# Performance work log

Hardware: AMD Instinct MI355X
Metric: run time of the kernel (lower is better)

Reference implementation:

```python
import jax, jax.numpy as jnp
import numpy as np

D_MODEL = 768
D_FF = 3072
N_HEADS = 12
HEAD_DIM = D_MODEL // N_HEADS
SUB_SCALE = 0.5
LN_EPS = 1e-5


def _layer_norm(x, g, b):
    mu = jnp.mean(x, axis=-1, keepdims=True)
    var = jnp.var(x, axis=-1, keepdims=True)
    return (x - mu) * jax.lax.rsqrt(var + LN_EPS) * g + b


def setup_inputs() -> dict:
    key = jax.random.key(0)
    ks = jax.random.split(key, 12)
    B, T = 1, 4096
    s = lambda fan_in: 1.0 / np.sqrt(fan_in)
    return {
        "x": jax.random.normal(ks[0], (B, T, D_MODEL), dtype=jnp.float32),
        "ln1_g": jnp.ones((D_MODEL,), jnp.float32),
        "ln1_b": jnp.zeros((D_MODEL,), jnp.float32),
        "ln2_g": jnp.ones((D_MODEL,), jnp.float32),
        "ln2_b": jnp.zeros((D_MODEL,), jnp.float32),
        "qkv_w": jax.random.normal(ks[1], (D_MODEL, 3 * D_MODEL), jnp.float32) * s(D_MODEL),
        "qkv_b": jnp.zeros((3 * D_MODEL,), jnp.float32),
        "out_w": jax.random.normal(ks[2], (D_MODEL, D_MODEL), jnp.float32) * s(D_MODEL),
        "out_b": jnp.zeros((D_MODEL,), jnp.float32),
        "fc1_w": jax.random.normal(ks[3], (D_MODEL, D_FF), jnp.float32) * s(D_MODEL),
        "fc1_b": jnp.zeros((D_FF,), jnp.float32),
        "fc2_w": jax.random.normal(ks[4], (D_FF, D_MODEL), jnp.float32) * s(D_FF),
        "fc2_b": jnp.zeros((D_MODEL,), jnp.float32),
    }


def reference(x, ln1_g, ln1_b, ln2_g, ln2_b, qkv_w, qkv_b, out_w, out_b,
              fc1_w, fc1_b, fc2_w, fc2_b):
    B, T, C = x.shape
    # --- attention sub-block ---
    h = _layer_norm(x, ln1_g, ln1_b) * SUB_SCALE
    qkv = h @ qkv_w + qkv_b                      # [B,T,3C]
    q, k, v = jnp.split(qkv, 3, axis=-1)
    split = lambda t: t.reshape(B, T, N_HEADS, HEAD_DIM).transpose(0, 2, 1, 3)
    q, k, v = split(q), split(k), split(v)       # [B,H,T,Hd]
    scores = jnp.einsum('bhqd,bhkd->bhqk', q, k) / jnp.sqrt(jnp.float32(HEAD_DIM))
    weights = jax.nn.softmax(scores, axis=-1)    # [B,H,T,T] (no mask, as in source)
    attn = jnp.einsum('bhqk,bhkd->bhqd', weights, v)
    attn = attn.transpose(0, 2, 1, 3).reshape(B, T, C)
    x = x + attn @ out_w + out_b
    # --- MLP sub-block ---
    h2 = _layer_norm(x, ln2_g, ln2_b) * SUB_SCALE
    h2 = jax.nn.gelu(h2 @ fc1_w + fc1_b, approximate=False)  # nn.GELU() = exact erf
    h2 = h2 @ fc2_w + fc2_b
    return x + h2
```

## Files before the change

kernel.cpp:

```cpp
#include <hip/hip_runtime.h>
#include <hip/hip_bf16.h>
#include <math.h>

#define TSEQ 4096
#define DMODEL 768
#define DFF 3072
#define NHEADS 12
#define HDIM 64

typedef __attribute__((ext_vector_type(8))) short short8;
typedef __attribute__((ext_vector_type(4))) float f32x4;
typedef unsigned short ushort;
typedef unsigned int uint;

typedef __attribute__((address_space(1))) ushort as1_ushort;
typedef __attribute__((address_space(3))) ushort as3_ushort;

__device__ __forceinline__ void gl_lds16(const ushort* g, const ushort* l) {
    __builtin_amdgcn_global_load_lds((as1_ushort*)(uintptr_t)g,
                                     (as3_ushort*)(uint)(uintptr_t)l, 16, 0, 0);
}

__device__ __forceinline__ ushort f2bf(float f) {
    union { float f; unsigned i; } c; c.f = f;
    unsigned x = c.i;
    unsigned r = x + 0x7FFFu + ((x >> 16) & 1u);
    return (ushort)(r >> 16);
}
__device__ __forceinline__ float asf(uint u) {
    union { unsigned i; float f; } c; c.i = u; return c.f;
}
__device__ __forceinline__ float gelu_fast(float v) {
    float y = v * (0.7978845608f + 0.03567740814f * v * v);
    float u = exp2f(y * -2.8853900817779268f);
    float r;
    asm("v_rcp_f32 %0, %1" : "=v"(r) : "v"(1.f + u));
    return v * r;
}

__global__ __launch_bounds__(256) void ln_half_kernel(
    const float* __restrict__ x, const float* __restrict__ g,
    const float* __restrict__ b, ushort* __restrict__ out)
{
    int row = blockIdx.x;
    const float* xr = x + (size_t)row * DMODEL;
    float v[3];
    float s = 0.f, s2 = 0.f;
    #pragma unroll
    for (int i = 0; i < 3; i++) {
        v[i] = xr[threadIdx.x + 256 * i];
        s += v[i]; s2 += v[i] * v[i];
    }
    #pragma unroll
    for (int m = 1; m < 64; m <<= 1) { s += __shfl_xor(s, m, 64); s2 += __shfl_xor(s2, m, 64); }
    __shared__ float ss[4], ss2[4];
    int wid = threadIdx.x >> 6;
    if ((threadIdx.x & 63) == 0) { ss[wid] = s; ss2[wid] = s2; }
    __syncthreads();
    s = ss[0] + ss[1] + ss[2] + ss[3];
    s2 = ss2[0] + ss2[1] + ss2[2] + ss2[3];
    float mu = s * (1.f / DMODEL);
    float var = s2 * (1.f / DMODEL) - mu * mu;
    float rs = rsqrtf(var + 1e-5f);
    #pragma unroll
    for (int i = 0; i < 3; i++) {
        int c = threadIdx.x + 256 * i;
        float h = (v[i] - mu) * rs * g[c] + b[c];
        out[(size_t)row * DMODEL + c] = f2bf(h * 0.5f);
    }
}

__global__ __launch_bounds__(256) void transpose_cast_kernel(
    const float* __restrict__ in, ushort* __restrict__ out, int K, int N)
{
    __shared__ float tile[32][33];
    int k0 = blockIdx.x * 32, n0 = blockIdx.y * 32;
    int c = threadIdx.x & 31, r0 = threadIdx.x >> 5;
    #pragma unroll
    for (int i = 0; i < 4; i++) {
        int r = r0 + i * 8;
        tile[r][c] = in[(size_t)(k0 + r) * N + n0 + c];
    }
    __syncthreads();
    #pragma unroll
    for (int i = 0; i < 4; i++) {
        int r = r0 + i * 8;
        out[(size_t)(n0 + r) * K + k0 + c] = f2bf(tile[c][r]);
    }
}

template<int EPI>
__global__ __launch_bounds__(256) void gemm_kernel(
    const ushort* __restrict__ A, const ushort* __restrict__ Bt,
    const float* __restrict__ bias, const float* __restrict__ res,
    void* __restrict__ out, ushort* __restrict__ vTout, int M, int N, int K)
{
    __shared__ ushort As[2][128 * 32];
    __shared__ ushort Bs[2][128 * 32];
    int bm = blockIdx.x * 128, bn = blockIdx.y * 128;
    int tid = threadIdx.x;
    int wid = tid >> 6, lane = tid & 63;
    int wm = (wid >> 1) * 64, wn = (wid & 1) * 64;
    int lg = lane >> 4, lr = lane & 15;
    int srow = lane >> 2, scol = (lane & 3) * 8;
    f32x4 acc[4][4] = {};

    const ushort* ga0 = A  + (size_t)(bm + wid * 16 + srow) * K + scol;
    const ushort* ga1 = A  + (size_t)(bm + 64 + wid * 16 + srow) * K + scol;
    const ushort* gb0 = Bt + (size_t)(bn + wid * 16 + srow) * K + scol;
    const ushort* gb1 = Bt + (size_t)(bn + 64 + wid * 16 + srow) * K + scol;

    gl_lds16(ga0, &As[0][wid * 512]);
    gl_lds16(ga1, &As[0][2048 + wid * 512]);
    gl_lds16(gb0, &Bs[0][wid * 512]);
    gl_lds16(gb1, &Bs[0][2048 + wid * 512]);

    int nt = K >> 5;
    for (int t = 0; t < nt; t++) {
        int cur = t & 1;
        __syncthreads();
        if (t + 1 < nt) {
            int k0 = (t + 1) << 5;
            int nb = cur ^ 1;
            gl_lds16(ga0 + k0, &As[nb][wid * 512]);
            gl_lds16(ga1 + k0, &As[nb][2048 + wid * 512]);
            gl_lds16(gb0 + k0, &Bs[nb][wid * 512]);
            gl_lds16(gb1 + k0, &Bs[nb][2048 + wid * 512]);
        }
        short8 a[4], b[4];
        #pragma unroll
        for (int mi = 0; mi < 4; mi++) a[mi] = *(const short8*)&As[cur][(wm + mi * 16 + lr) * 32 + lg * 8];
        #pragma unroll
        for (int ni = 0; ni < 4; ni++) b[ni] = *(const short8*)&Bs[cur][(wn + ni * 16 + lr) * 32 + lg * 8];
        #pragma unroll
        for (int mi = 0; mi < 4; mi++)
            #pragma unroll
            for (int ni = 0; ni < 4; ni++)
                acc[mi][ni] = __builtin_amdgcn_mfma_f32_16x16x32_bf16(a[mi], b[ni], acc[mi][ni], 0, 0, 0);
    }

    #pragma unroll
    for (int mi = 0; mi < 4; mi++) {
        #pragma unroll
        for (int ni = 0; ni < 4; ni++) {
            int col = bn + wn + ni * 16 + lr;
            float bv = bias[col];
            if (EPI == 3 && bn >= 1536) {
                int row0 = bm + wm + mi * 16 + lg * 4;
                uint2 pk;
                pk.x = (uint)f2bf(acc[mi][ni][0] + bv) | ((uint)f2bf(acc[mi][ni][1] + bv) << 16);
                pk.y = (uint)f2bf(acc[mi][ni][2] + bv) | ((uint)f2bf(acc[mi][ni][3] + bv) << 16);
                *(uint2*)&vTout[(size_t)(col - 1536) * TSEQ + row0] = pk;
            } else {
                #pragma unroll
                for (int r = 0; r < 4; r++) {
                    int row = bm + wm + mi * 16 + lg * 4 + r;
                    float v = acc[mi][ni][r] + bv;
                    size_t idx = (size_t)row * N + col;
                    if (EPI == 1) {
                        ((ushort*)out)[idx] = f2bf(gelu_fast(v));
                    } else if (EPI == 2) {
                        ((float*)out)[idx] = v + res[idx];
                    } else {
                        ((ushort*)out)[idx] = f2bf(v);
                    }
                }
            }
        }
    }
}

template<int EPI>
__global__ __launch_bounds__(256) void gemm_64_kernel(
    const ushort* __restrict__ A, const ushort* __restrict__ Bt,
    const float* __restrict__ bias, const float* __restrict__ res,
    void* __restrict__ out, int M, int N, int K)
{
    __shared__ ushort As[2][64 * 32];
    __shared__ ushort Bs[2][64 * 32];
    int bm = blockIdx.x * 64, bn = blockIdx.y * 64;
    int tid = threadIdx.x;
    int wid = tid >> 6, lane = tid & 63;
    int wm = (wid >> 1) * 32, wn = (wid & 1) * 32;
    int lg = lane >> 4, lr = lane & 15;
    int srow = tid >> 2;
    int sunit = (tid & 3) ^ (srow & 3);
    f32x4 acc[2][2] = {};

    const ushort* ga = A  + (size_t)(bm + srow) * K + sunit * 8;
    const ushort* gb = Bt + (size_t)(bn + srow) * K + sunit * 8;

    gl_lds16(ga, &As[0][tid * 8]);
    gl_lds16(gb, &Bs[0][tid * 8]);

    int nt = K >> 5;
    for (int t = 0; t < nt; t++) {
        int cur = t & 1;
        __syncthreads();
        if (t + 1 < nt) {
            int k0 = (t + 1) << 5;
            int nb = cur ^ 1;
            gl_lds16(ga + k0, &As[nb][tid * 8]);
            gl_lds16(gb + k0, &Bs[nb][tid * 8]);
        }
        short8 a[2], b[2];
        #pragma unroll
        for (int mi = 0; mi < 2; mi++) {
            int row = wm + mi * 16 + lr;
            a[mi] = *(const short8*)&As[cur][row * 32 + ((lg ^ (row & 3)) * 8)];
        }
        #pragma unroll
        for (int ni = 0; ni < 2; ni++) {
            int row = wn + ni * 16 + lr;
            b[ni] = *(const short8*)&Bs[cur][row * 32 + ((lg ^ (row & 3)) * 8)];
        }
        #pragma unroll
        for (int mi = 0; mi < 2; mi++)
            #pragma unroll
            for (int ni = 0; ni < 2; ni++)
                acc[mi][ni] = __builtin_amdgcn_mfma_f32_16x16x32_bf16(a[mi], b[ni], acc[mi][ni], 0, 0, 0);
    }

    #pragma unroll
    for (int mi = 0; mi < 2; mi++) {
        #pragma unroll
        for (int ni = 0; ni < 2; ni++) {
            int col = bn + wn + ni * 16 + lr;
            float bv = bias[col];
            #pragma unroll
            for (int r = 0; r < 4; r++) {
                int row = bm + wm + mi * 16 + lg * 4 + r;
                float v = acc[mi][ni][r] + bv;
                size_t idx = (size_t)row * N + col;
                if (EPI == 0) {
                    ((ushort*)out)[idx] = f2bf(v);
                } else if (EPI == 1) {
                    ((ushort*)out)[idx] = f2bf(gelu_fast(v));
                } else {
                    ((float*)out)[idx] = v + res[idx];
                }
            }
        }
    }
}

__global__ __launch_bounds__(512) void attn_kernel(
    const ushort* __restrict__ qkv, const ushort* __restrict__ vT,
    ushort* __restrict__ Opart, float* __restrict__ ml)
{
    int combo = blockIdx.x % 48;
    int qblk  = blockIdx.x / 48;
    int h     = combo >> 2;
    int split = combo & 3;
    __shared__ ushort smem[16384 + 256 * 40];
    ushort* Ps = smem + 16384;
    int tid = threadIdx.x, wid = tid >> 6, lane = tid & 63;
    int lg = lane >> 4, lr = lane & 15;
    const float C1 = 0.18033688011112042f;
    const float KC = 12.0f * C1;
    int x7 = lr & 7;

    {
        int row = tid >> 1;
        int u0 = (tid & 1) * 4;
        int r7 = row & 7;
        const ushort* src = qkv + (size_t)(qblk * 256 + row) * 2304 + h * HDIM;
        #pragma unroll
        for (int i = 0; i < 4; i++) {
            int u = u0 + i;
            *(short8*)&smem[row * 64 + ((u ^ r7) * 8)] = *(const short8*)(src + (size_t)(u * 8));
        }
    }
    int q0row = (wid * 32 + lr) * 64;
    int q1row = q0row + 16 * 64;
    short8 qa0 = *(const short8*)&smem[q0row + (lg ^ x7) * 8];
    short8 qa1 = *(const short8*)&smem[q0row + ((4 + lg) ^ x7) * 8];
    short8 qb0 = *(const short8*)&smem[q1row + (lg ^ x7) * 8];
    short8 qb1 = *(const short8*)&smem[q1row + ((4 + lg) ^ x7) * 8];
    __syncthreads();

    short8 vone;
    #pragma unroll
    for (int i = 0; i < 8; i++) vone[i] = (short)0x3F80;

    int krow = tid >> 3;
    int kunit = (tid & 7) ^ (krow & 7);
    const ushort* kg = qkv + (size_t)(split * 1024 + krow) * 2304 + DMODEL + h * HDIM + kunit * 8;
    const ushort* vgp = vT + (size_t)(h * HDIM + krow) * TSEQ + split * 1024 + kunit * 8;

    gl_lds16(kg, &smem[tid * 8]);
    gl_lds16(vgp, &smem[8192 + tid * 8]);
    kg += 64 * 2304;
    vgp += 64;

    f32x4 o0[4] = {}, o1[4] = {};
    f32x4 s0sum = {}, s1sum = {};
    const int NT = 16;
    int prow0 = (wid * 32 + lr) * 40;
    int prow1 = prow0 + 16 * 40;

    for (int kt = 0; kt < NT; kt++) {
        int cur = kt & 1, nb = cur ^ 1;
        __syncthreads();
        if (kt + 1 < NT) {
            gl_lds16(kg, &smem[nb * 4096 + tid * 8]);
            gl_lds16(vgp, &smem[8192 + nb * 4096 + tid * 8]);
            kg += 64 * 2304;
            vgp += 64;
        }
        const ushort* kb = &smem[cur * 4096];
        const ushort* vb = &smem[8192 + cur * 4096];

        f32x4 st0[4] = {}, st1[4] = {};
        __builtin_amdgcn_s_setprio(1);
        #pragma unroll
        for (int ki = 0; ki < 4; ki++) {
            const ushort* kr = &kb[(ki * 16 + lr) * 64];
            short8 k0 = *(const short8*)&kr[(lg ^ x7) * 8];
            short8 k1 = *(const short8*)&kr[((4 + lg) ^ x7) * 8];
            st0[ki] = __builtin_amdgcn_mfma_f32_16x16x32_bf16(k0, qa0, st0[ki], 0, 0, 0);
            st0[ki] = __builtin_amdgcn_mfma_f32_16x16x32_bf16(k1, qa1, st0[ki], 0, 0, 0);
            st1[ki] = __builtin_amdgcn_mfma_f32_16x16x32_bf16(k0, qb0, st1[ki], 0, 0, 0);
            st1[ki] = __builtin_amdgcn_mfma_f32_16x16x32_bf16(k1, qb1, st1[ki], 0, 0, 0);
        }
        __builtin_amdgcn_s_setprio(0);

        uint2 c0[4], c1[4];
        #pragma unroll
        for (int ki = 0; ki < 4; ki++) {
            #pragma unroll
            for (int r = 0; r < 4; r++) st0[ki][r] = exp2f(st0[ki][r] * C1 - KC);
            asm("v_cvt_pk_bf16_f32 %0, %1, %2" : "=v"(c0[ki].x) : "v"(st0[ki][0]), "v"(st0[ki][1]));
            asm("v_cvt_pk_bf16_f32 %0, %1, %2" : "=v"(c0[ki].y) : "v"(st0[ki][2]), "v"(st0[ki][3]));
        }
        #pragma unroll
        for (int ki = 0; ki < 4; ki++) {
            #pragma unroll
            for (int r = 0; r < 4; r++) st1[ki][r] = exp2f(st1[ki][r] * C1 - KC);
            asm("v_cvt_pk_bf16_f32 %0, %1, %2" : "=v"(c1[ki].x) : "v"(st1[ki][0]), "v"(st1[ki][1]));
            asm("v_cvt_pk_bf16_f32 %0, %1, %2" : "=v"(c1[ki].y) : "v"(st1[ki][2]), "v"(st1[ki][3]));
        }

        *(uint2*)&Ps[prow0 + lg * 4]      = c0[0];
        *(uint2*)&Ps[prow0 + 16 + lg * 4] = c0[1];
        *(uint2*)&Ps[prow1 + lg * 4]      = c1[0];
        *(uint2*)&Ps[prow1 + 16 + lg * 4] = c1[1];
        {
            short8 pa00 = *(const short8*)&Ps[prow0 + lg * 8];
            short8 pa10 = *(const short8*)&Ps[prow1 + lg * 8];
            __builtin_amdgcn_s_setprio(1);
            s0sum = __builtin_amdgcn_mfma_f32_16x16x32_bf16(pa00, vone, s0sum, 0, 0, 0);
            s1sum = __builtin_amdgcn_mfma_f32_16x16x32_bf16(pa10, vone, s1sum, 0, 0, 0);
            #pragma unroll
            for (int ni = 0; ni < 4; ni++) {
                short8 b0 = *(const short8*)&vb[(ni * 16 + lr) * 64 + (lg ^ x7) * 8];
                o0[ni] = __builtin_amdgcn_mfma_f32_16x16x32_bf16(pa00, b0, o0[ni], 0, 0, 0);
                o1[ni] = __builtin_amdgcn_mfma_f32_16x16x32_bf16(pa10, b0, o1[ni], 0, 0, 0);
            }
            __builtin_amdgcn_s_setprio(0);
        }
        *(uint2*)&Ps[prow0 + lg * 4]      = c0[2];
        *(uint2*)&Ps[prow0 + 16 + lg * 4] = c0[3];
        *(uint2*)&Ps[prow1 + lg * 4]      = c1[2];
        *(uint2*)&Ps[prow1 + 16 + lg * 4] = c1[3];
        {
            short8 pa01 = *(const short8*)&Ps[prow0 + lg * 8];
            short8 pa11 = *(const short8*)&Ps[prow1 + lg * 8];
            __builtin_amdgcn_s_setprio(1);
            s0sum = __builtin_amdgcn_mfma_f32_16x16x32_bf16(pa01, vone, s0sum, 0, 0, 0);
            s1sum = __builtin_amdgcn_mfma_f32_16x16x32_bf16(pa11, vone, s1sum, 0, 0, 0);
            #pragma unroll
            for (int ni = 0; ni < 4; ni++) {
                short8 b1 = *(const short8*)&vb[(ni * 16 + lr) * 64 + ((4 + lg) ^ x7) * 8];
                o0[ni] = __builtin_amdgcn_mfma_f32_16x16x32_bf16(pa01, b1, o0[ni], 0, 0, 0);
                o1[ni] = __builtin_amdgcn_mfma_f32_16x16x32_bf16(pa11, b1, o1[ni], 0, 0, 0);
            }
            __builtin_amdgcn_s_setprio(0);
        }
    }

    if (lr == 0) {
        #pragma unroll
        for (int r = 0; r < 4; r++) {
            int q0 = qblk * 256 + wid * 32 + lg * 4 + r;
            ml[((size_t)split * NHEADS + h) * TSEQ + q0]      = s0sum[r];
            ml[((size_t)split * NHEADS + h) * TSEQ + q0 + 16] = s1sum[r];
        }
    }
    #pragma unroll
    for (int ni = 0; ni < 4; ni++)
        #pragma unroll
        for (int r = 0; r < 4; r++) {
            int q0 = qblk * 256 + wid * 32 + lg * 4 + r;
            int dcol = ni * 16 + lr;
            Opart[((size_t)split * TSEQ + q0) * DMODEL + h * HDIM + dcol]      = f2bf(o0[ni][r]);
            Opart[((size_t)split * TSEQ + q0 + 16) * DMODEL + h * HDIM + dcol] = f2bf(o1[ni][r]);
        }
}

__global__ __launch_bounds__(256) void attn_combine_kernel(
    const ushort* __restrict__ Opart, const float* __restrict__ ml,
    ushort* __restrict__ attnb)
{
    int gid = blockIdx.x * 256 + threadIdx.x;
    int q = gid / 192;
    int c = (gid - q * 192) * 4;
    int hh = c >> 6;
    float denom = 0.f;
    float a0 = 0.f, a1 = 0.f, a2 = 0.f, a3 = 0.f;
    #pragma unroll
    for (int s = 0; s < 4; s++) {
        denom += ml[((size_t)s * NHEADS + hh) * TSEQ + q];
        uint2 ov = *(const uint2*)&Opart[((size_t)s * TSEQ + q) * DMODEL + c];
        a0 += asf(ov.x << 16);
        a1 += asf(ov.x & 0xFFFF0000u);
        a2 += asf(ov.y << 16);
        a3 += asf(ov.y & 0xFFFF0000u);
    }
    float rd = 1.f / denom;
    uint2 stv;
    stv.x = (uint)f2bf(a0 * rd) | ((uint)f2bf(a1 * rd) << 16);
    stv.y = (uint)f2bf(a2 * rd) | ((uint)f2bf(a3 * rd) << 16);
    *(uint2*)&attnb[(size_t)q * DMODEL + c] = stv;
}

extern "C" void kernel_launch(void* const* d_in, const int* in_sizes, int n_in,
                              void* d_out, int out_size, void* d_ws, size_t ws_size,
                              hipStream_t stream)
{
    const float* x      = (const float*)d_in[0];
    const float* ln1_g  = (const float*)d_in[1];
    const float* ln1_b  = (const float*)d_in[2];
    const float* ln2_g  = (const float*)d_in[3];
    const float* ln2_b  = (const float*)d_in[4];
    const float* qkv_w  = (const float*)d_in[5];
    const float* qkv_b  = (const float*)d_in[6];
    const float* out_w  = (const float*)d_in[7];
    const float* out_b  = (const float*)d_in[8];
    const float* fc1_w  = (const float*)d_in[9];
    const float* fc1_b  = (const float*)d_in[10];
    const float* fc2_w  = (const float*)d_in[11];
    const float* fc2_b  = (const float*)d_in[12];
    (void)in_sizes; (void)n_in; (void)out_size; (void)ws_size;

    char* p = (char*)d_ws;
    ushort* qkvb  = (ushort*)p;                 p += (size_t)TSEQ * DFF * 2;
    ushort* hb    = (ushort*)p;                 p += (size_t)TSEQ * DMODEL * 2;
    ushort* attnb = (ushort*)p;                 p += (size_t)TSEQ * DMODEL * 2;
    float*  x2    = (float*)p;                  p += (size_t)TSEQ * DMODEL * 4;
    ushort* qkv_wT = (ushort*)p;                p += (size_t)(3 * DMODEL) * DMODEL * 2;
    ushort* out_wT = (ushort*)p;                p += (size_t)DMODEL * DMODEL * 2;
    ushort* fc1_wT = (ushort*)p;                p += (size_t)DFF * DMODEL * 2;
    ushort* fc2_wT = (ushort*)p;                p += (size_t)DMODEL * DFF * 2;
    ushort* Opart  = (ushort*)p;                p += (size_t)4 * TSEQ * DMODEL * 2;
    float*  mlbuf  = (float*)p;                 p += (size_t)4 * NHEADS * TSEQ * 4;
    ushort* vTb    = (ushort*)p;                p += (size_t)DMODEL * TSEQ * 2;
    ushort* gb = qkvb;

    transpose_cast_kernel<<<dim3(DMODEL / 32, 3 * DMODEL / 32), 256, 0, stream>>>(qkv_w, qkv_wT, DMODEL, 3 * DMODEL);
    transpose_cast_kernel<<<dim3(DMODEL / 32, DMODEL / 32), 256, 0, stream>>>(out_w, out_wT, DMODEL, DMODEL);
    transpose_cast_kernel<<<dim3(DMODEL / 32, DFF / 32), 256, 0, stream>>>(fc1_w, fc1_wT, DMODEL, DFF);
    transpose_cast_kernel<<<dim3(DFF / 32, DMODEL / 32), 256, 0, stream>>>(fc2_w, fc2_wT, DFF, DMODEL);

    ln_half_kernel<<<TSEQ, 256, 0, stream>>>(x, ln1_g, ln1_b, hb);
    gemm_kernel<3><<<dim3(TSEQ / 128, 3 * DMODEL / 128), 256, 0, stream>>>(
        hb, qkv_wT, qkv_b, nullptr, qkvb, vTb, TSEQ, 3 * DMODEL, DMODEL);
    attn_kernel<<<dim3((TSEQ / 256) * NHEADS * 4), 512, 0, stream>>>(qkvb, vTb, Opart, mlbuf);
    attn_combine_kernel<<<(TSEQ * DMODEL / 4) / 256, 256, 0, stream>>>(Opart, mlbuf, attnb);
    gemm_64_kernel<2><<<dim3(TSEQ / 64, DMODEL / 64), 256, 0, stream>>>(
        attnb, out_wT, out_b, x, x2, TSEQ, DMODEL, DMODEL);
    ln_half_kernel<<<TSEQ, 256, 0, stream>>>(x2, ln2_g, ln2_b, hb);
    gemm_kernel<1><<<dim3(TSEQ / 128, DFF / 128), 256, 0, stream>>>(
        hb, fc1_wT, fc1_b, nullptr, gb, nullptr, TSEQ, DFF, DMODEL);
    gemm_64_kernel<2><<<dim3(TSEQ / 64, DMODEL / 64), 256, 0, stream>>>(
        gb, fc2_wT, fc2_b, x2, (float*)d_out, TSEQ, DMODEL, DFF);
}
```

Before: 212.2 us.

## Use 64x128 GEMM tiles with XOR-swizzled LDS layout for QKV and FC1

Replaces the 128x128 GEMM tile with a 64x128 tile for the QKV and FC1 projections, doubling the block count so more CUs are filled on a 4096-row problem. It also adds an XOR swizzle on the 16-byte unit index when staging into LDS and when reading fragments, to cut LDS bank conflicts on the fragment reads. The unused residual epilogue is removed. The trade-off is less register-level reuse per wave (2x4 MFMA fragments instead of 4x4) and more total global traffic for the B operand.

```diff
diff --git a/kernel.cpp b/kernel.cpp
--- a/kernel.cpp
+++ b/kernel.cpp
@@ -90,30 +90,31 @@
 }
 
 template<int EPI>
-__global__ __launch_bounds__(256) void gemm_kernel(
+__global__ __launch_bounds__(256) void gemm_6428_kernel(
     const ushort* __restrict__ A, const ushort* __restrict__ Bt,
-    const float* __restrict__ bias, const float* __restrict__ res,
+    const float* __restrict__ bias,
     void* __restrict__ out, ushort* __restrict__ vTout, int M, int N, int K)
 {
-    __shared__ ushort As[2][128 * 32];
+    __shared__ ushort As[2][64 * 32];
     __shared__ ushort Bs[2][128 * 32];
-    int bm = blockIdx.x * 128, bn = blockIdx.y * 128;
+    int bm = blockIdx.x * 64, bn = blockIdx.y * 128;
     int tid = threadIdx.x;
     int wid = tid >> 6, lane = tid & 63;
-    int wm = (wid >> 1) * 64, wn = (wid & 1) * 64;
+    int wm = (wid >> 1) * 32, wn = (wid & 1) * 64;
     int lg = lane >> 4, lr = lane & 15;
-    int srow = lane >> 2, scol = (lane & 3) * 8;
-    f32x4 acc[4][4] = {};
-
-    const ushort* ga0 = A  + (size_t)(bm + wid * 16 + srow) * K + scol;
-    const ushort* ga1 = A  + (size_t)(bm + 64 + wid * 16 + srow) * K + scol;
-    const ushort* gb0 = Bt + (size_t)(bn + wid * 16 + srow) * K + scol;
-    const ushort* gb1 = Bt + (size_t)(bn + 64 + wid * 16 + srow) * K + scol;
-
-    gl_lds16(ga0, &As[0][wid * 512]);
-    gl_lds16(ga1, &As[0][2048 + wid * 512]);
-    gl_lds16(gb0, &Bs[0][wid * 512]);
-    gl_lds16(gb1, &Bs[0][2048 + wid * 512]);
+    f32x4 acc[2][4] = {};
+
+    int sarow = tid >> 2;
+    int saunit = (tid & 3) ^ (sarow & 3);
+    const ushort* ga = A + (size_t)(bm + sarow) * K + saunit * 8;
+    int sbrow0 = wid * 16 + (lane >> 2);
+    int sbunit = (lane & 3) ^ ((lane >> 2) & 3);
+    const ushort* gb0 = Bt + (size_t)(bn + sbrow0) * K + sbunit * 8;
+    const ushort* gb1 = Bt + (size_t)(bn + 64 + sbrow0) * K + sbunit * 8;
+
+    gl_lds16(ga,  &As[0][tid * 8]);
+    gl_lds16(gb0, &Bs[0][tid * 8]);
+    gl_lds16(gb1, &Bs[0][2048 + tid * 8]);
 
     int nt = K >> 5;
     for (int t = 0; t < nt; t++) {
@@ -122,25 +123,30 @@
         if (t + 1 < nt) {
             int k0 = (t + 1) << 5;
             int nb = cur ^ 1;
-            gl_lds16(ga0 + k0, &As[nb][wid * 512]);
-            gl_lds16(ga1 + k0, &As[nb][2048 + wid * 512]);
-            gl_lds16(gb0 + k0, &Bs[nb][wid * 512]);
-            gl_lds16(gb1 + k0, &Bs[nb][2048 + wid * 512]);
-        }
-        short8 a[4], b[4];
-        #pragma unroll
-        for (int mi = 0; mi < 4; mi++) a[mi] = *(const short8*)&As[cur][(wm + mi * 16 + lr) * 32 + lg * 8];
-        #pragma unroll
-        for (int ni = 0; ni < 4; ni++) b[ni] = *(const short8*)&Bs[cur][(wn + ni * 16 + lr) * 32 + lg * 8];
-        #pragma unroll
-        for (int mi = 0; mi < 4; mi++)
+            gl_lds16(ga + k0,  &As[nb][tid * 8]);
+            gl_lds16(gb0 + k0, &Bs[nb][tid * 8]);
+            gl_lds16(gb1 + k0, &Bs[nb][2048 + tid * 8]);
+        }
+        short8 a[2], b[4];
+        #pragma unroll
+        for (int mi = 0; mi < 2; mi++) {
+            int row = wm + mi * 16 + lr;
+            a[mi] = *(const short8*)&As[cur][row * 32 + ((lg ^ (row & 3)) * 8)];
+        }
+        #pragma unroll
+        for (int ni = 0; ni < 4; ni++) {
+            int row = wn + ni * 16 + lr;
+            b[ni] = *(const short8*)&Bs[cur][row * 32 + ((lg ^ (row & 3)) * 8)];
+        }
+        #pragma unroll
+        for (int mi = 0; mi < 2; mi++)
             #pragma unroll
             for (int ni = 0; ni < 4; ni++)
                 acc[mi][ni] = __builtin_amdgcn_mfma_f32_16x16x32_bf16(a[mi], b[ni], acc[mi][ni], 0, 0, 0);
     }
 
     #pragma unroll
-    for (int mi = 0; mi < 4; mi++) {
+    for (int mi = 0; mi < 2; mi++) {
         #pragma unroll
         for (int ni = 0; ni < 4; ni++) {
             int col = bn + wn + ni * 16 + lr;
@@ -159,8 +165,6 @@
                     size_t idx = (size_t)row * N + col;
                     if (EPI == 1) {
                         ((ushort*)out)[idx] = f2bf(gelu_fast(v));
-                    } else if (EPI == 2) {
-                        ((float*)out)[idx] = v + res[idx];
                     } else {
                         ((ushort*)out)[idx] = f2bf(v);
                     }
@@ -463,15 +467,15 @@
     transpose_cast_kernel<<<dim3(DFF / 32, DMODEL / 32), 256, 0, stream>>>(fc2_w, fc2_wT, DFF, DMODEL);
 
     ln_half_kernel<<<TSEQ, 256, 0, stream>>>(x, ln1_g, ln1_b, hb);
-    gemm_kernel<3><<<dim3(TSEQ / 128, 3 * DMODEL / 128), 256, 0, stream>>>(
-        hb, qkv_wT, qkv_b, nullptr, qkvb, vTb, TSEQ, 3 * DMODEL, DMODEL);
+    gemm_6428_kernel<3><<<dim3(TSEQ / 64, 3 * DMODEL / 128), 256, 0, stream>>>(
+        hb, qkv_wT, qkv_b, qkvb, vTb, TSEQ, 3 * DMODEL, DMODEL);
     attn_kernel<<<dim3((TSEQ / 256) * NHEADS * 4), 512, 0, stream>>>(qkvb, vTb, Opart, mlbuf);
     attn_combine_kernel<<<(TSEQ * DMODEL / 4) / 256, 256, 0, stream>>>(Opart, mlbuf, attnb);
     gemm_64_kernel<2><<<dim3(TSEQ / 64, DMODEL / 64), 256, 0, stream>>>(
         attnb, out_wT, out_b, x, x2, TSEQ, DMODEL, DMODEL);
     ln_half_kernel<<<TSEQ, 256, 0, stream>>>(x2, ln2_g, ln2_b, hb);
-    gemm_kernel<1><<<dim3(TSEQ / 128, DFF / 128), 256, 0, stream>>>(
-        hb, fc1_wT, fc1_b, nullptr, gb, nullptr, TSEQ, DFF, DMODEL);
+    gemm_6428_kernel<1><<<dim3(TSEQ / 64, DFF / 128), 256, 0, stream>>>(
+        hb, fc1_wT, fc1_b, gb, nullptr, TSEQ, DFF, DMODEL);
     gemm_64_kernel<2><<<dim3(TSEQ / 64, DMODEL / 64), 256, 0, stream>>>(
         gb, fc2_wT, fc2_b, x2, (float*)d_out, TSEQ, DMODEL, DFF);
 }
```

Result: slower. 223.2 us (+5.2%).
